# Kernel tuning notes

Hardware: AMD Instinct MI355X
Metric: run time of the kernel (lower is better)

Reference implementation:

```python
import jax, jax.numpy as jnp
import numpy as np

UNITS = 512
SENSORY = 256
BATCH = 256
ODE_UNFOLDS = 6
EPSILON = 1e-8
ELAPSED_TIME = 1.0


def setup_inputs() -> dict:
    key = jax.random.key(0)
    ks = jax.random.split(key, 16)
    u = lambda k, shape, lo, hi: jax.random.uniform(k, shape, jnp.float32, lo, hi)
    pm1 = lambda k, shape: (jax.random.randint(k, shape, 0, 2).astype(jnp.float32) * 2.0 - 1.0)
    return {
        "x": jax.random.normal(ks[0], (BATCH, SENSORY), jnp.float32),
        "state": jax.random.normal(ks[1], (BATCH, UNITS), jnp.float32),
        "gleak": u(ks[2], (UNITS,), 0.001, 1.0),
        "vleak": u(ks[3], (UNITS,), -0.2, 0.2),
        "cm": u(ks[4], (UNITS,), 0.4, 0.6),
        "sigma": u(ks[5], (UNITS, UNITS), 3.0, 8.0),
        "mu": u(ks[6], (UNITS, UNITS), 0.3, 0.8),
        "w": u(ks[7], (UNITS, UNITS), 0.001, 1.0),
        "erev": pm1(ks[8], (UNITS, UNITS)),
        "sensory_sigma": u(ks[9], (SENSORY, UNITS), 3.0, 8.0),
        "sensory_mu": u(ks[10], (SENSORY, UNITS), 0.3, 0.8),
        "sensory_w": u(ks[11], (SENSORY, UNITS), 0.001, 1.0),
        "sensory_erev": pm1(ks[12], (SENSORY, UNITS)),
        "input_w": jnp.ones((SENSORY,), jnp.float32),
        "input_b": jnp.zeros((SENSORY,), jnp.float32),
        "output_w": jnp.ones((UNITS,), jnp.float32),
        "output_b": jnp.zeros((UNITS,), jnp.float32),
    }


def _gate(v_pre, mu, sigma):
    # v_pre: (B, P) broadcast against (P, Q) params -> (B, P, Q)
    return jax.nn.sigmoid(sigma * (v_pre[:, :, None] - mu))


def reference(x, state, gleak, vleak, cm, sigma, mu, w, erev,
              sensory_sigma, sensory_mu, sensory_w, sensory_erev,
              input_w, input_b, output_w, output_b):
    inputs = x * input_w + input_b  # (B, D)
    sens_act = sensory_w * _gate(inputs, sensory_mu, sensory_sigma)  # (B, D, N)
    w_num_sensory = jnp.sum(sens_act * sensory_erev, axis=1)  # (B, N)
    w_den_sensory = jnp.sum(sens_act, axis=1)                 # (B, N)

    cm_t = cm / ((ELAPSED_TIME + 0.001) / ODE_UNFOLDS)  # (N,)
    v_pre = state
    for _ in range(ODE_UNFOLDS):
        w_act = w * _gate(v_pre, mu, sigma)               # (B, N, N)
        w_num = jnp.sum(w_act * erev, axis=1) + w_num_sensory
        w_den = jnp.sum(w_act, axis=1) + w_den_sensory
        numerator = cm_t * v_pre + gleak * vleak + w_num
        denominator = cm_t + gleak + w_den
        v_pre = numerator / (denominator + EPSILON)

    outputs = v_pre * output_w + output_b
    return outputs, v_pre
```

## Files before the change

kernel.cpp:

```cpp
#include <hip/hip_runtime.h>

#define UNITS 512
#define SENSD 256
#define BATCH 256
#define BN (BATCH * UNITS)
#define LOG2E 1.44269504088896340736f
#define CMF (6.0f / 1.001f)

__device__ __forceinline__ float frcp(float x)  { return __builtin_amdgcn_rcpf(x); }
__device__ __forceinline__ float fexp2(float x) { return __builtin_amdgcn_exp2f(x); }

__global__ __launch_bounds__(256) void prep_kernel(
    const float* __restrict__ sigma, const float* __restrict__ mu,
    const float* __restrict__ w, const float* __restrict__ erev,
    const float* __restrict__ ssig, const float* __restrict__ smu,
    const float* __restrict__ sw, const float* __restrict__ serev,
    const float* __restrict__ gleak, const float* __restrict__ vleak,
    const float* __restrict__ cm,
    float4* __restrict__ fusedR, float4* __restrict__ fusedS,
    float4* __restrict__ cmg) {
  int idx = blockIdx.x * 256 + threadIdx.x;
  if (idx < UNITS * UNITS) {
    float s = sigma[idx], m = mu[idx], ww = w[idx], e = erev[idx];
    fusedR[idx] = make_float4(-s * LOG2E, s * m * LOG2E, ww, ww * e);
  } else {
    int j = idx - UNITS * UNITS;
    if (j < SENSD * UNITS) {
      float s = ssig[j], m = smu[j], ww = sw[j], e = serev[j];
      fusedS[j] = make_float4(-s * LOG2E, s * m * LOG2E, ww, ww * e);
    }
  }
  if (idx < UNITS) {
    float cmt = cm[idx] * CMF, gl = gleak[idx];
    cmg[idx] = make_float4(cmt, gl * vleak[idx], cmt + gl + 1e-8f, 0.f);
  }
}

__global__ __launch_bounds__(256) void sensory_kernel(
    const float* __restrict__ x, const float* __restrict__ in_w, const float* __restrict__ in_b,
    const float4* __restrict__ fusedS,
    float* __restrict__ snf, float* __restrict__ sdf) {
  __shared__ float xl[8][128];
  int bi = blockIdx.x;
  int phs = bi & 1, qt = (bi >> 1) & 7, bt = bi >> 4;
  int tid = threadIdx.x;
  for (int i = tid; i < 8 * 128; i += 256) {
    int br = i >> 7, dl = i & 127;
    int d = phs * 128 + dl;
    xl[br][dl] = fmaf(x[(bt * 8 + br) * SENSD + d], in_w[d], in_b[d]);
  }
  __syncthreads();
  int ql = tid & 63, bg = tid >> 6;
  int q = qt * 64 + ql;
  int r0 = bg * 2;
  const float4* F = fusedS + (size_t)(phs * 128) * UNITS + q;
  float n0 = 0.f, dn0 = 0.f, n1 = 0.f, dn1 = 0.f;
  #pragma unroll 8
  for (int dd = 0; dd < 128; ++dd) {
    float4 f = F[(size_t)dd * UNITS];
    float v0 = xl[r0][dd], v1 = xl[r0 + 1][dd];
    float t0 = fexp2(fmaf(f.x, v0, f.y));
    float t1 = fexp2(fmaf(f.x, v1, f.y));
    float s0 = frcp(1.0f + t0);
    float s1 = frcp(1.0f + t1);
    n0 = fmaf(f.w, s0, n0);  dn0 = fmaf(f.z, s0, dn0);
    n1 = fmaf(f.w, s1, n1);  dn1 = fmaf(f.z, s1, dn1);
  }
  int b0 = bt * 8 + r0;
  int bp0 = b0 * UNITS + q, bp1 = bp0 + UNITS;
  snf[bp0 * 2 + phs] = n0;  sdf[bp0 * 2 + phs] = dn0;
  snf[bp1 * 2 + phs] = n1;  sdf[bp1 * 2 + phs] = dn1;
}

__global__ __launch_bounds__(512, 4) void unfold_kernel(
    const float4* __restrict__ fusedR, const float* __restrict__ vprev,
    const float4* __restrict__ pn_in, const float4* __restrict__ pd_in,
    const float* __restrict__ snf, const float* __restrict__ sdf,
    const float4* __restrict__ cmg,
    float* __restrict__ vout,
    float* __restrict__ pn_out, float* __restrict__ pd_out,
    int first) {
  __shared__ float vl[16][128];
  int bi = blockIdx.x;
  int ph = bi & 3, qt = (bi >> 2) & 7, bt = bi >> 5;
  int tid = threadIdx.x;
  if (first) {
    for (int i = tid; i < 2048; i += 512) {
      int br = i >> 7, pl = i & 127;
      vl[br][pl] = vprev[(bt * 16 + br) * UNITS + ph * 128 + pl];
    }
  } else {
    for (int i = tid; i < 2048; i += 512) {
      int br = i >> 7, pl = i & 127;
      int p = ph * 128 + pl;
      int bp = (bt * 16 + br) * UNITS + p;
      float4 a = pn_in[bp], b = pd_in[bp];
      float2 s2 = *(const float2*)&snf[bp * 2];
      float2 d2 = *(const float2*)&sdf[bp * 2];
      float num = (a.x + a.y) + (a.z + a.w) + (s2.x + s2.y);
      float den = (b.x + b.y) + (b.z + b.w) + (d2.x + d2.y);
      float4 c = cmg[p];
      float v = fmaf(c.x, vprev[bp], c.y + num) * frcp(c.z + den);
      vl[br][pl] = v;
      if (qt == 0) vout[bp] = v;
    }
  }
  __syncthreads();
  int ql = tid & 63, bg = tid >> 6;
  int q = qt * 64 + ql;
  int r0 = bg * 2;
  const float4* F = fusedR + (size_t)(ph * 128) * UNITS + q;
  float n0 = 0.f, dn0 = 0.f, n1 = 0.f, dn1 = 0.f;
  #pragma unroll 8
  for (int pp = 0; pp < 128; ++pp) {
    float4 f = F[(size_t)pp * UNITS];
    float v0 = vl[r0][pp], v1 = vl[r0 + 1][pp];
    float t0 = fexp2(fmaf(f.x, v0, f.y));
    float t1 = fexp2(fmaf(f.x, v1, f.y));
    float s0 = frcp(1.0f + t0);
    float s1 = frcp(1.0f + t1);
    n0 = fmaf(f.w, s0, n0);  dn0 = fmaf(f.z, s0, dn0);
    n1 = fmaf(f.w, s1, n1);  dn1 = fmaf(f.z, s1, dn1);
  }
  int b0 = bt * 16 + r0;
  int bp0 = b0 * UNITS + q, bp1 = bp0 + UNITS;
  pn_out[bp0 * 4 + ph] = n0;  pd_out[bp0 * 4 + ph] = dn0;
  pn_out[bp1 * 4 + ph] = n1;  pd_out[bp1 * 4 + ph] = dn1;
}

__global__ __launch_bounds__(256) void final_kernel(
    const float* __restrict__ vprev,
    const float4* __restrict__ pn, const float4* __restrict__ pd,
    const float* __restrict__ snf, const float* __restrict__ sdf,
    const float4* __restrict__ cmg,
    const float* __restrict__ ow, const float* __restrict__ ob,
    float* __restrict__ out) {
  int idx = blockIdx.x * 256 + threadIdx.x;
  if (idx >= BN) return;
  int p = idx & (UNITS - 1);
  float4 a = pn[idx], b = pd[idx];
  float2 s2 = *(const float2*)&snf[idx * 2];
  float2 d2 = *(const float2*)&sdf[idx * 2];
  float num = (a.x + a.y) + (a.z + a.w) + (s2.x + s2.y);
  float den = (b.x + b.y) + (b.z + b.w) + (d2.x + d2.y);
  float4 c = cmg[p];
  float v = fmaf(c.x, vprev[idx], c.y + num) * frcp(c.z + den);
  out[idx] = fmaf(v, ow[p], ob[p]);
  out[BN + idx] = v;
}

extern "C" void kernel_launch(void* const* d_in, const int* in_sizes, int n_in,
                              void* d_out, int out_size, void* d_ws, size_t ws_size,
                              hipStream_t stream) {
  (void)in_sizes; (void)n_in; (void)out_size; (void)ws_size;
  const float* x     = (const float*)d_in[0];
  const float* state = (const float*)d_in[1];
  const float* gleak = (const float*)d_in[2];
  const float* vleak = (const float*)d_in[3];
  const float* cm    = (const float*)d_in[4];
  const float* sigma = (const float*)d_in[5];
  const float* mu    = (const float*)d_in[6];
  const float* w     = (const float*)d_in[7];
  const float* erev  = (const float*)d_in[8];
  const float* ssig  = (const float*)d_in[9];
  const float* smu   = (const float*)d_in[10];
  const float* sw    = (const float*)d_in[11];
  const float* serev = (const float*)d_in[12];
  const float* in_w  = (const float*)d_in[13];
  const float* in_b  = (const float*)d_in[14];
  const float* out_w = (const float*)d_in[15];
  const float* out_b = (const float*)d_in[16];

  float* ws = (float*)d_ws;
  float4* fusedR = (float4*)(ws);
  float4* fusedS = (float4*)(ws + 1048576);
  float4* cmg    = (float4*)(ws + 1572864);
  float4* pnA    = (float4*)(ws + 1574912);
  float4* pdA    = (float4*)(ws + 2099200);
  float4* pnB    = (float4*)(ws + 2623488);
  float4* pdB    = (float4*)(ws + 3147776);
  float*  snf    = ws + 3672064;
  float*  sdf    = ws + 3934208;
  float*  vA     = ws + 4196352;
  float*  vB     = ws + 4327424;

  prep_kernel<<<1536, 256, 0, stream>>>(sigma, mu, w, erev, ssig, smu, sw, serev,
                                        gleak, vleak, cm, fusedR, fusedS, cmg);
  sensory_kernel<<<512, 256, 0, stream>>>(x, in_w, in_b, fusedS, snf, sdf);

  unfold_kernel<<<512, 512, 0, stream>>>(fusedR, state, pnA, pdA, snf, sdf, cmg,
                                         vA, (float*)pnA, (float*)pdA, 1);
  unfold_kernel<<<512, 512, 0, stream>>>(fusedR, state, pnA, pdA, snf, sdf, cmg,
                                         vA, (float*)pnB, (float*)pdB, 0);
  unfold_kernel<<<512, 512, 0, stream>>>(fusedR, vA, pnB, pdB, snf, sdf, cmg,
                                         vB, (float*)pnA, (float*)pdA, 0);
  unfold_kernel<<<512, 512, 0, stream>>>(fusedR, vB, pnA, pdA, snf, sdf, cmg,
                                         vA, (float*)pnB, (float*)pdB, 0);
  unfold_kernel<<<512, 512, 0, stream>>>(fusedR, vA, pnB, pdB, snf, sdf, cmg,
                                         vB, (float*)pnA, (float*)pdA, 0);
  unfold_kernel<<<512, 512, 0, stream>>>(fusedR, vB, pnA, pdA, snf, sdf, cmg,
                                         vA, (float*)pnB, (float*)pdB, 0);
  final_kernel<<<512, 256, 0, stream>>>(vA, pnB, pdB, snf, sdf, cmg,
                                        out_w, out_b, (float*)d_out);
}
```

Baseline: 164.7 us.

## Compute four batch rows per thread and store partial sums phase-major

Each thread in the sensory and unfold kernels now accumulates four batch rows instead of two. Each fused parameter float4 loaded from global memory is therefore reused across more rows, and the block size is halved to 256 threads. The shared-memory tile is transposed so one float4 LDS read fetches the four row values. Partial-sum buffers move from interleaved per-element layout to phase-major planes, which makes stores and reloads coalesced. The cost is more registers per thread and fewer waves per block, which can reduce latency hiding.

```diff
diff --git a/kernel.cpp b/kernel.cpp
--- a/kernel.cpp
+++ b/kernel.cpp
@@ -36,101 +36,118 @@
   }
 }
 
-__global__ __launch_bounds__(256) void sensory_kernel(
+__global__ __launch_bounds__(256, 2) void sensory_kernel(
     const float* __restrict__ x, const float* __restrict__ in_w, const float* __restrict__ in_b,
     const float4* __restrict__ fusedS,
     float* __restrict__ snf, float* __restrict__ sdf) {
-  __shared__ float xl[8][128];
+  __shared__ float xl[128][20];
   int bi = blockIdx.x;
   int phs = bi & 1, qt = (bi >> 1) & 7, bt = bi >> 4;
   int tid = threadIdx.x;
-  for (int i = tid; i < 8 * 128; i += 256) {
+  for (int i = tid; i < 2048; i += 256) {
     int br = i >> 7, dl = i & 127;
     int d = phs * 128 + dl;
-    xl[br][dl] = fmaf(x[(bt * 8 + br) * SENSD + d], in_w[d], in_b[d]);
+    xl[dl][br] = fmaf(x[(bt * 16 + br) * SENSD + d], in_w[d], in_b[d]);
   }
   __syncthreads();
   int ql = tid & 63, bg = tid >> 6;
   int q = qt * 64 + ql;
-  int r0 = bg * 2;
+  int r0 = bg * 4;
   const float4* F = fusedS + (size_t)(phs * 128) * UNITS + q;
-  float n0 = 0.f, dn0 = 0.f, n1 = 0.f, dn1 = 0.f;
+  float n0 = 0.f, n1 = 0.f, n2 = 0.f, n3 = 0.f;
+  float d0 = 0.f, d1 = 0.f, d2 = 0.f, d3 = 0.f;
   #pragma unroll 8
   for (int dd = 0; dd < 128; ++dd) {
     float4 f = F[(size_t)dd * UNITS];
-    float v0 = xl[r0][dd], v1 = xl[r0 + 1][dd];
-    float t0 = fexp2(fmaf(f.x, v0, f.y));
-    float t1 = fexp2(fmaf(f.x, v1, f.y));
+    float4 vv = *(const float4*)&xl[dd][r0];
+    float t0 = fexp2(fmaf(f.x, vv.x, f.y));
+    float t1 = fexp2(fmaf(f.x, vv.y, f.y));
+    float t2 = fexp2(fmaf(f.x, vv.z, f.y));
+    float t3 = fexp2(fmaf(f.x, vv.w, f.y));
     float s0 = frcp(1.0f + t0);
     float s1 = frcp(1.0f + t1);
-    n0 = fmaf(f.w, s0, n0);  dn0 = fmaf(f.z, s0, dn0);
-    n1 = fmaf(f.w, s1, n1);  dn1 = fmaf(f.z, s1, dn1);
-  }
-  int b0 = bt * 8 + r0;
-  int bp0 = b0 * UNITS + q, bp1 = bp0 + UNITS;
-  snf[bp0 * 2 + phs] = n0;  sdf[bp0 * 2 + phs] = dn0;
-  snf[bp1 * 2 + phs] = n1;  sdf[bp1 * 2 + phs] = dn1;
-}
-
-__global__ __launch_bounds__(512, 4) void unfold_kernel(
+    float s2 = frcp(1.0f + t2);
+    float s3 = frcp(1.0f + t3);
+    n0 = fmaf(f.w, s0, n0);  d0 = fmaf(f.z, s0, d0);
+    n1 = fmaf(f.w, s1, n1);  d1 = fmaf(f.z, s1, d1);
+    n2 = fmaf(f.w, s2, n2);  d2 = fmaf(f.z, s2, d2);
+    n3 = fmaf(f.w, s3, n3);  d3 = fmaf(f.z, s3, d3);
+  }
+  int bp = (bt * 16 + r0) * UNITS + q;
+  size_t o = (size_t)phs * BN + bp;
+  snf[o] = n0;             sdf[o] = d0;
+  snf[o + UNITS] = n1;     sdf[o + UNITS] = d1;
+  snf[o + 2 * UNITS] = n2; sdf[o + 2 * UNITS] = d2;
+  snf[o + 3 * UNITS] = n3; sdf[o + 3 * UNITS] = d3;
+}
+
+__global__ __launch_bounds__(256, 2) void unfold_kernel(
     const float4* __restrict__ fusedR, const float* __restrict__ vprev,
-    const float4* __restrict__ pn_in, const float4* __restrict__ pd_in,
+    const float* __restrict__ pn_in, const float* __restrict__ pd_in,
     const float* __restrict__ snf, const float* __restrict__ sdf,
     const float4* __restrict__ cmg,
     float* __restrict__ vout,
     float* __restrict__ pn_out, float* __restrict__ pd_out,
     int first) {
-  __shared__ float vl[16][128];
+  __shared__ float vl[128][20];
   int bi = blockIdx.x;
   int ph = bi & 3, qt = (bi >> 2) & 7, bt = bi >> 5;
   int tid = threadIdx.x;
   if (first) {
-    for (int i = tid; i < 2048; i += 512) {
+    for (int i = tid; i < 2048; i += 256) {
       int br = i >> 7, pl = i & 127;
-      vl[br][pl] = vprev[(bt * 16 + br) * UNITS + ph * 128 + pl];
+      vl[pl][br] = vprev[(bt * 16 + br) * UNITS + ph * 128 + pl];
     }
   } else {
-    for (int i = tid; i < 2048; i += 512) {
+    for (int i = tid; i < 2048; i += 256) {
       int br = i >> 7, pl = i & 127;
       int p = ph * 128 + pl;
       int bp = (bt * 16 + br) * UNITS + p;
-      float4 a = pn_in[bp], b = pd_in[bp];
-      float2 s2 = *(const float2*)&snf[bp * 2];
-      float2 d2 = *(const float2*)&sdf[bp * 2];
-      float num = (a.x + a.y) + (a.z + a.w) + (s2.x + s2.y);
-      float den = (b.x + b.y) + (b.z + b.w) + (d2.x + d2.y);
+      float num = ((pn_in[bp] + pn_in[BN + bp]) + (pn_in[2 * BN + bp] + pn_in[3 * BN + bp]))
+                + (snf[bp] + snf[BN + bp]);
+      float den = ((pd_in[bp] + pd_in[BN + bp]) + (pd_in[2 * BN + bp] + pd_in[3 * BN + bp]))
+                + (sdf[bp] + sdf[BN + bp]);
       float4 c = cmg[p];
       float v = fmaf(c.x, vprev[bp], c.y + num) * frcp(c.z + den);
-      vl[br][pl] = v;
+      vl[pl][br] = v;
       if (qt == 0) vout[bp] = v;
     }
   }
   __syncthreads();
   int ql = tid & 63, bg = tid >> 6;
   int q = qt * 64 + ql;
-  int r0 = bg * 2;
+  int r0 = bg * 4;
   const float4* F = fusedR + (size_t)(ph * 128) * UNITS + q;
-  float n0 = 0.f, dn0 = 0.f, n1 = 0.f, dn1 = 0.f;
+  float n0 = 0.f, n1 = 0.f, n2 = 0.f, n3 = 0.f;
+  float d0 = 0.f, d1 = 0.f, d2 = 0.f, d3 = 0.f;
   #pragma unroll 8
   for (int pp = 0; pp < 128; ++pp) {
     float4 f = F[(size_t)pp * UNITS];
-    float v0 = vl[r0][pp], v1 = vl[r0 + 1][pp];
-    float t0 = fexp2(fmaf(f.x, v0, f.y));
-    float t1 = fexp2(fmaf(f.x, v1, f.y));
+    float4 vv = *(const float4*)&vl[pp][r0];
+    float t0 = fexp2(fmaf(f.x, vv.x, f.y));
+    float t1 = fexp2(fmaf(f.x, vv.y, f.y));
+    float t2 = fexp2(fmaf(f.x, vv.z, f.y));
+    float t3 = fexp2(fmaf(f.x, vv.w, f.y));
     float s0 = frcp(1.0f + t0);
     float s1 = frcp(1.0f + t1);
-    n0 = fmaf(f.w, s0, n0);  dn0 = fmaf(f.z, s0, dn0);
-    n1 = fmaf(f.w, s1, n1);  dn1 = fmaf(f.z, s1, dn1);
-  }
-  int b0 = bt * 16 + r0;
-  int bp0 = b0 * UNITS + q, bp1 = bp0 + UNITS;
-  pn_out[bp0 * 4 + ph] = n0;  pd_out[bp0 * 4 + ph] = dn0;
-  pn_out[bp1 * 4 + ph] = n1;  pd_out[bp1 * 4 + ph] = dn1;
+    float s2 = frcp(1.0f + t2);
+    float s3 = frcp(1.0f + t3);
+    n0 = fmaf(f.w, s0, n0);  d0 = fmaf(f.z, s0, d0);
+    n1 = fmaf(f.w, s1, n1);  d1 = fmaf(f.z, s1, d1);
+    n2 = fmaf(f.w, s2, n2);  d2 = fmaf(f.z, s2, d2);
+    n3 = fmaf(f.w, s3, n3);  d3 = fmaf(f.z, s3, d3);
+  }
+  int bp = (bt * 16 + r0) * UNITS + q;
+  size_t o = (size_t)ph * BN + bp;
+  pn_out[o] = n0;             pd_out[o] = d0;
+  pn_out[o + UNITS] = n1;     pd_out[o + UNITS] = d1;
+  pn_out[o + 2 * UNITS] = n2; pd_out[o + 2 * UNITS] = d2;
+  pn_out[o + 3 * UNITS] = n3; pd_out[o + 3 * UNITS] = d3;
 }
 
 __global__ __launch_bounds__(256) void final_kernel(
     const float* __restrict__ vprev,
-    const float4* __restrict__ pn, const float4* __restrict__ pd,
+    const float* __restrict__ pn, const float* __restrict__ pd,
     const float* __restrict__ snf, const float* __restrict__ sdf,
     const float4* __restrict__ cmg,
     const float* __restrict__ ow, const float* __restrict__ ob,
@@ -138,11 +155,10 @@
   int idx = blockIdx.x * 256 + threadIdx.x;
   if (idx >= BN) return;
   int p = idx & (UNITS - 1);
-  float4 a = pn[idx], b = pd[idx];
-  float2 s2 = *(const float2*)&snf[idx * 2];
-  float2 d2 = *(const float2*)&sdf[idx * 2];
-  float num = (a.x + a.y) + (a.z + a.w) + (s2.x + s2.y);
-  float den = (b.x + b.y) + (b.z + b.w) + (d2.x + d2.y);
+  float num = ((pn[idx] + pn[BN + idx]) + (pn[2 * BN + idx] + pn[3 * BN + idx]))
+            + (snf[idx] + snf[BN + idx]);
+  float den = ((pd[idx] + pd[BN + idx]) + (pd[2 * BN + idx] + pd[3 * BN + idx]))
+            + (sdf[idx] + sdf[BN + idx]);
   float4 c = cmg[p];
   float v = fmaf(c.x, vprev[idx], c.y + num) * frcp(c.z + den);
   out[idx] = fmaf(v, ow[p], ob[p]);
@@ -175,10 +191,10 @@
   float4* fusedR = (float4*)(ws);
   float4* fusedS = (float4*)(ws + 1048576);
   float4* cmg    = (float4*)(ws + 1572864);
-  float4* pnA    = (float4*)(ws + 1574912);
-  float4* pdA    = (float4*)(ws + 2099200);
-  float4* pnB    = (float4*)(ws + 2623488);
-  float4* pdB    = (float4*)(ws + 3147776);
+  float*  pnA    = ws + 1574912;
+  float*  pdA    = ws + 2099200;
+  float*  pnB    = ws + 2623488;
+  float*  pdB    = ws + 3147776;
   float*  snf    = ws + 3672064;
   float*  sdf    = ws + 3934208;
   float*  vA     = ws + 4196352;
@@ -186,20 +202,20 @@
 
   prep_kernel<<<1536, 256, 0, stream>>>(sigma, mu, w, erev, ssig, smu, sw, serev,
                                         gleak, vleak, cm, fusedR, fusedS, cmg);
-  sensory_kernel<<<512, 256, 0, stream>>>(x, in_w, in_b, fusedS, snf, sdf);
-
-  unfold_kernel<<<512, 512, 0, stream>>>(fusedR, state, pnA, pdA, snf, sdf, cmg,
-                                         vA, (float*)pnA, (float*)pdA, 1);
-  unfold_kernel<<<512, 512, 0, stream>>>(fusedR, state, pnA, pdA, snf, sdf, cmg,
-                                         vA, (float*)pnB, (float*)pdB, 0);
-  unfold_kernel<<<512, 512, 0, stream>>>(fusedR, vA, pnB, pdB, snf, sdf, cmg,
-                                         vB, (float*)pnA, (float*)pdA, 0);
-  unfold_kernel<<<512, 512, 0, stream>>>(fusedR, vB, pnA, pdA, snf, sdf, cmg,
-                                         vA, (float*)pnB, (float*)pdB, 0);
-  unfold_kernel<<<512, 512, 0, stream>>>(fusedR, vA, pnB, pdB, snf, sdf, cmg,
-                                         vB, (float*)pnA, (float*)pdA, 0);
-  unfold_kernel<<<512, 512, 0, stream>>>(fusedR, vB, pnA, pdA, snf, sdf, cmg,
-                                         vA, (float*)pnB, (float*)pdB, 0);
+  sensory_kernel<<<256, 256, 0, stream>>>(x, in_w, in_b, fusedS, snf, sdf);
+
+  unfold_kernel<<<512, 256, 0, stream>>>(fusedR, state, pnA, pdA, snf, sdf, cmg,
+                                         vA, pnA, pdA, 1);
+  unfold_kernel<<<512, 256, 0, stream>>>(fusedR, state, pnA, pdA, snf, sdf, cmg,
+                                         vA, pnB, pdB, 0);
+  unfold_kernel<<<512, 256, 0, stream>>>(fusedR, vA, pnB, pdB, snf, sdf, cmg,
+                                         vB, pnA, pdA, 0);
+  unfold_kernel<<<512, 256, 0, stream>>>(fusedR, vB, pnA, pdA, snf, sdf, cmg,
+                                         vA, pnB, pdB, 0);
+  unfold_kernel<<<512, 256, 0, stream>>>(fusedR, vA, pnB, pdB, snf, sdf, cmg,
+                                         vB, pnA, pdA, 0);
+  unfold_kernel<<<512, 256, 0, stream>>>(fusedR, vB, pnA, pdA, snf, sdf, cmg,
+                                         vA, pnB, pdB, 0);
   final_kernel<<<512, 256, 0, stream>>>(vA, pnB, pdB, snf, sdf, cmg,
                                         out_w, out_b, (float*)d_out);
 }
```

Result: slower. 196.4 us (+19.3%).
